# Kernel optimization log

Hardware: AMD Instinct MI355X
Metric: run time of the kernel (lower is better)

Reference implementation:

```python
import jax, jax.numpy as jnp
import numpy as np
from jax import lax

P_SIZE = 3
STRIDE = 1
PAD = 0
ANCILLA = 1
NQ = P_SIZE * P_SIZE + ANCILLA  # 10 qubits -> 1024-dim statevector


def _circuit_last_z(pv, theta):
    """Simulated quantum circuit on a batch of patches.

    pv:    [P, 9] patch pixel values used as RY encoding angles
    theta: [NQ]   fixed circuit parameters (trainBool=False)
    Returns <Z> of the last (ancilla) qubit: [P, 1].
    """
    P = pv.shape[0]
    # ancilla qubit(s) appended with angle 0 (|0> state), as in QuantumKernel
    angles = jnp.concatenate([pv, jnp.zeros((P, ANCILLA), pv.dtype)], axis=-1)  # [P, NQ]

    # angle-encoding product state: RY(a_q)|0> = [cos(a/2), sin(a/2)] per qubit
    state = jnp.ones((P, 1), pv.dtype)
    for q in range(NQ):
        half = angles[:, q] * 0.5
        amp = jnp.stack([jnp.cos(half), jnp.sin(half)], axis=-1)  # [P, 2]
        state = (state[:, :, None] * amp[:, None, :]).reshape(P, -1)
    # state: [P, 2**NQ], qubit 0 is most-significant bit

    # chain-graph entanglement: CNOT(q -> q+1)
    for q in range(NQ - 1):
        s = state.reshape(P, 2 ** q, 2, 2, -1)  # [P, L, ctrl, tgt, R]
        state = jnp.stack([s[:, :, 0], s[:, :, 1, ::-1]], axis=2).reshape(P, -1)

    # fixed parameterized RY layer (all-real gates keep statevector real)
    for q in range(NQ):
        h = theta[q] * 0.5
        c, sn = jnp.cos(h), jnp.sin(h)
        G = jnp.stack([jnp.stack([c, -sn]), jnp.stack([sn, c])])  # [2, 2]
        st = state.reshape(P, 2 ** q, 2, -1)
        state = jnp.einsum('ij,pljr->plir', G, st).reshape(P, -1)

    probs = state * state
    pq = probs.reshape(P, 2 ** (NQ - 1), 2)  # last qubit is least-significant
    z_last = pq[:, :, 0].sum(axis=1) - pq[:, :, 1].sum(axis=1)
    return z_last[:, None]  # channels_out = [-1]


def setup_inputs() -> dict:
    key = jax.random.key(0)
    kx, kt = jax.random.split(key)
    x = jax.random.normal(kx, (16, 3, 64, 64), dtype=jnp.float32)
    theta = jax.random.normal(kt, (NQ,), dtype=jnp.float32)
    return {"x": x, "theta": theta}


def reference(x, theta):
    B, C, H, W = x.shape
    Ho = (H + 2 * PAD - P_SIZE) // STRIDE + 1
    Wo = (W + 2 * PAD - P_SIZE) // STRIDE + 1
    outs = []
    for c in range(C):  # per-channel loop, mirrors the torch module
        # im2col / unfold: [B, 9, Ho, Wo], kernel flattened row-major like nn.Unfold
        patches = lax.conv_general_dilated_patches(
            x[:, c:c + 1], (P_SIZE, P_SIZE), (STRIDE, STRIDE),
            [(PAD, PAD), (PAD, PAD)])
        pv = patches.reshape(B, P_SIZE * P_SIZE, Ho * Wo)
        pv = pv.transpose(0, 2, 1).reshape(-1, P_SIZE * P_SIZE)  # [B*Ho*Wo, 9]
        ko = _circuit_last_z(pv, theta)                           # [B*Ho*Wo, 1]
        ko = ko.reshape(B, Ho * Wo, 1).transpose(0, 2, 1)
        outs.append(ko.reshape(B, 1, Ho, Wo))
    return jnp.concatenate(outs, axis=1)  # [B, C, Ho, Wo]
```

## Files before the change

kernel.cpp:

```cpp
#include <hip/hip_runtime.h>


#define BB 16
#define CC 3
#define HH 64
#define WW 64
#define HO 62
#define WO 62

__global__ __launch_bounds__(256) void qconv_closed_form(
    const float* __restrict__ x,
    const float* __restrict__ theta,
    float* __restrict__ out)
{
    const int total = BB * CC * HO * WO;
    int idx = blockIdx.x * blockDim.x + threadIdx.x;
    if (idx >= total) return;

    int j  = idx % WO;
    int t  = idx / WO;
    int i  = t % HO;
    int bc = t / HO;

    const float ct9 = __cosf(theta[9]);

    const float* xp = x + (bc * HH + i) * WW + j;
    float p = ct9;
#pragma unroll
    for (int di = 0; di < 3; ++di) {
        const float* r = xp + di * WW;
        p *= __cosf(r[0]);
        p *= __cosf(r[1]);
        p *= __cosf(r[2]);
    }
    out[idx] = p;
}

extern "C" void kernel_launch(void* const* d_in, const int* in_sizes, int n_in,
                              void* d_out, int out_size, void* d_ws, size_t ws_size,
                              hipStream_t stream) {
    const float* x     = (const float*)d_in[0];
    const float* theta = (const float*)d_in[1];
    float* out         = (float*)d_out;

    const int total = BB * CC * HO * WO;
    const int block = 256;
    const int grid  = (total + block - 1) / block;
    qconv_closed_form<<<grid, block, 0, stream>>>(x, theta, out);
}
```

Baseline: 55.09 us.

## Compute 2x2 output block per thread reusing shared cosine products

Each thread now loads a 4x4 input window and produces a 2x2 block of outputs, so cosines and partial row and column products are shared across neighbouring outputs instead of being recomputed nine times per output. Outputs are written as float2 pairs. This cuts transcendental and load work and the thread count by about four, at the cost of fewer threads in flight and float2 stores at 8-byte-aligned offsets, which rely on even output row width.

```diff
diff --git a/kernel.cpp b/kernel.cpp
--- a/kernel.cpp
+++ b/kernel.cpp
@@ -7,33 +7,48 @@
 #define WW 64
 #define HO 62
 #define WO 62
+#define QD 31
+#define NTH (BB * CC * QD * QD)
 
-__global__ __launch_bounds__(256) void qconv_closed_form(
+__global__ __launch_bounds__(256) void qconv_quad(
     const float* __restrict__ x,
     const float* __restrict__ theta,
     float* __restrict__ out)
 {
-    const int total = BB * CC * HO * WO;
-    int idx = blockIdx.x * blockDim.x + threadIdx.x;
-    if (idx >= total) return;
+    int tid = blockIdx.x * blockDim.x + threadIdx.x;
+    if (tid >= NTH) return;
 
-    int j  = idx % WO;
-    int t  = idx / WO;
-    int i  = t % HO;
-    int bc = t / HO;
+    int qj = tid % QD;
+    int t  = tid / QD;
+    int qi = t % QD;
+    int bc = t / QD;
+    int i = qi * 2, j = qj * 2;
 
     const float ct9 = __cosf(theta[9]);
 
     const float* xp = x + (bc * HH + i) * WW + j;
-    float p = ct9;
+
+    float p0[4], p1[4];
 #pragma unroll
-    for (int di = 0; di < 3; ++di) {
-        const float* r = xp + di * WW;
-        p *= __cosf(r[0]);
-        p *= __cosf(r[1]);
-        p *= __cosf(r[2]);
+    for (int r = 0; r < 4; ++r) {
+        const float* row = xp + r * WW;
+        float c0 = __cosf(row[0]);
+        float c1 = __cosf(row[1]);
+        float c2 = __cosf(row[2]);
+        float c3 = __cosf(row[3]);
+        float m  = c1 * c2;
+        p0[r] = c0 * m;
+        p1[r] = m * c3;
     }
-    out[idx] = p;
+
+    float q0 = p0[1] * p0[2] * ct9;
+    float q1 = p1[1] * p1[2] * ct9;
+
+    float* op = out + (bc * HO + i) * WO + j;
+    float2 o0 = make_float2(p0[0] * q0, p1[0] * q1);
+    float2 o1 = make_float2(q0 * p0[3], q1 * p1[3]);
+    *(float2*)(op)      = o0;
+    *(float2*)(op + WO) = o1;
 }
 
 extern "C" void kernel_launch(void* const* d_in, const int* in_sizes, int n_in,
@@ -43,8 +58,7 @@
     const float* theta = (const float*)d_in[1];
     float* out         = (float*)d_out;
 
-    const int total = BB * CC * HO * WO;
     const int block = 256;
-    const int grid  = (total + block - 1) / block;
-    qconv_closed_form<<<grid, block, 0, stream>>>(x, theta, out);
+    const int grid  = (NTH + block - 1) / block;
+    qconv_quad<<<grid, block, 0, stream>>>(x, theta, out);
 }
```

After: 54.70 us. Within noise of the previous version (-0.7%).
